# Optimization experiments

Measured on AMD Instinct MI355X. Metric: run time of the kernel, lower is better.

## Reference

```python
import jax, jax.numpy as jnp
import numpy as np

E = 1024   # embedding_size
H = 16     # num_heads
DH = E // H


def setup_inputs() -> dict:
    key = jax.random.key(0)
    ks = jax.random.split(key, 11)
    B, S = 2, 2048
    std = 0.02
    return {
        "query": jax.random.normal(ks[0], (B, S, E), jnp.float32),
        "key": jax.random.normal(ks[1], (B, S, E), jnp.float32),
        "value": jax.random.normal(ks[2], (B, S, E), jnp.float32),
        "Wq": jax.random.normal(ks[3], (E, E), jnp.float32) * std,
        "bq": jnp.zeros((E,), jnp.float32),
        "Wk": jax.random.normal(ks[4], (E, E), jnp.float32) * std,
        "bk": jnp.zeros((E,), jnp.float32),
        "Wv": jax.random.normal(ks[5], (E, E), jnp.float32) * std,
        "bv": jnp.zeros((E,), jnp.float32),
        "Wo": jax.random.normal(ks[6], (E, E), jnp.float32) * std,
        "bo": jnp.zeros((E,), jnp.float32),
    }


def _split_heads(x, B, S):
    # [B,S,E] -> [B,H,S,DH]
    return x.reshape(B, S, H, DH).transpose(0, 2, 1, 3)


def reference(query, key, value, Wq, bq, Wk, bk, Wv, bv, Wo, bo):
    B, S, _ = query.shape
    # torch Linear: y = x @ W.T + b
    q = _split_heads(query @ Wq.T + bq, B, S)
    k = _split_heads(key @ Wk.T + bk, B, key.shape[1])
    v = _split_heads(value @ Wv.T + bv, B, value.shape[1])
    # naive unscaled attention (original has no 1/sqrt(d) factor)
    scores = jnp.einsum("bhsd,bhtd->bhst", q, k)  # [B,H,S,T]
    attn = jax.nn.softmax(scores, axis=-1)
    out = jnp.einsum("bhst,bhtd->bhsd", attn, v)  # [B,H,S,DH]
    out = out.transpose(0, 2, 1, 3).reshape(B, S, E)
    return out @ Wo.T + bo
```

## Files before the change

### kernel.cpp

```cpp
#include <hip/hip_runtime.h>
#include <hip/hip_bf16.h>

constexpr int kB   = 2;
constexpr int kS   = 2048;
constexpr int kE   = 1024;
constexpr int kH   = 16;
constexpr int kDH  = 64;
constexpr int kTok = kB * kS;

constexpr float kLog2e = 1.4426950408889634f;

typedef short bf16x8 __attribute__((ext_vector_type(8)));
typedef float f32x4  __attribute__((ext_vector_type(4)));
typedef unsigned int uint2v __attribute__((ext_vector_type(2)));

__device__ __forceinline__ float bf2f(unsigned short s) {
  union { unsigned int u; float f; } c; c.u = ((unsigned int)s) << 16; return c.f;
}
__device__ __forceinline__ unsigned short f2bf(float f) {
  union { float f; unsigned int u; } c; c.f = f;
  unsigned int u = c.u;
  u += 0x7fffu + ((u >> 16) & 1u);
  return (unsigned short)(u >> 16);
}

__device__ __forceinline__ unsigned cvtpk(float lo, float hi) {
  unsigned r;
  asm("v_cvt_pk_bf16_f32 %0, %1, %2" : "=v"(r) : "v"(lo), "v"(hi));
  return r;
}

__device__ __forceinline__ float fexp2(float x) {
  float r;
  asm("v_exp_f32 %0, %1" : "=v"(r) : "v"(x));
  return r;
}

__device__ __forceinline__ void gl_lds16(const unsigned short* g, unsigned short* l) {
  __builtin_amdgcn_global_load_lds(
      (const __attribute__((address_space(1))) unsigned int*)g,
      (__attribute__((address_space(3))) unsigned int*)l, 16, 0, 0);
}

__global__ void detect_dtype(const unsigned short* __restrict__ q, int* flag) {
  __shared__ int cnt;
  if (threadIdx.x == 0) cnt = 0;
  __syncthreads();
  int bad = 0;
  for (int i = threadIdx.x; i < 4096; i += 256) {
    unsigned int e = (q[i] >> 7) & 0xFF;
    if (e >= 0xC0) bad++;
  }
  atomicAdd(&cnt, bad);
  __syncthreads();
  if (threadIdx.x == 0) *flag = (cnt > 8) ? 1 : 0;
}

struct Seg { const void* src; unsigned short* dst; unsigned int n; unsigned int blk0; };
struct ConvArgs { Seg s[11]; float scale[11]; };

__global__ __launch_bounds__(256) void conv_all(ConvArgs a, const int* __restrict__ flag) {
  const unsigned int bid = blockIdx.x;
  int si = 0;
  #pragma unroll
  for (int i = 1; i < 11; ++i)
    if (bid >= a.s[i].blk0) si = i;
  const Seg sg = a.s[si];
  const float sc = a.scale[si];
  const int i0 = ((int)(bid - sg.blk0) * 256 + threadIdx.x) * 8;
  if (i0 >= (int)sg.n) return;
  if (*flag) {
    const float* s = (const float*)sg.src + i0;
    f32x4 f0 = *(const f32x4*)(s);
    f32x4 f1 = *(const f32x4*)(s + 4);
    bf16x8 v;
    #pragma unroll
    for (int j = 0; j < 4; ++j) v[j]     = (short)f2bf(f0[j] * sc);
    #pragma unroll
    for (int j = 0; j < 4; ++j) v[j + 4] = (short)f2bf(f1[j] * sc);
    *(bf16x8*)&sg.dst[i0] = v;
  } else {
    bf16x8 v = *(const bf16x8*)((const unsigned short*)sg.src + i0);
    if (sc != 1.0f) {
      #pragma unroll
      for (int j = 0; j < 8; ++j)
        v[j] = (short)f2bf(bf2f((unsigned short)v[j]) * sc);
    }
    *(bf16x8*)&sg.dst[i0] = v;
  }
}

__device__ __forceinline__ void gemm_core(
    const unsigned short* __restrict__ A,
    const unsigned short* __restrict__ W,
    int Kdim, int bM, int bN,
    unsigned short* As, unsigned short* Ws,
    f32x4 acc[4][4])
{
  const int tid  = threadIdx.x;
  const int lane = tid & 63;
  const int wv   = tid >> 6;
  const int wm   = (wv >> 1) * 64;
  const int wn   = (wv & 1) * 64;
  const int lr   = lane & 15;
  const int kq   = (lane >> 4) * 8;

  const int r0 = tid >> 2;
  const int c0 = (tid & 3) * 8;

  const unsigned short* Ag = A + (size_t)(bM + r0) * Kdim + c0;
  const unsigned short* Wg = W + (size_t)(bN + r0) * Kdim + c0;
  unsigned short* lA = &As[tid * 8];
  unsigned short* lW = &Ws[tid * 8];

  for (int k0 = 0; k0 < Kdim; k0 += 32) {
    gl_lds16(Ag + k0,                      lA);
    gl_lds16(Ag + (size_t)64 * Kdim + k0,  lA + 2048);
    gl_lds16(Wg + k0,                      lW);
    gl_lds16(Wg + (size_t)64 * Kdim + k0,  lW + 2048);
    __syncthreads();

    bf16x8 a[4], b[4];
    #pragma unroll
    for (int i = 0; i < 4; ++i)
      a[i] = *(const bf16x8*)&As[(wm + i * 16 + lr) * 32 + kq];
    #pragma unroll
    for (int i = 0; i < 4; ++i)
      b[i] = *(const bf16x8*)&Ws[(wn + i * 16 + lr) * 32 + kq];
    #pragma unroll
    for (int i = 0; i < 4; ++i)
      #pragma unroll
      for (int j = 0; j < 4; ++j)
        acc[i][j] = __builtin_amdgcn_mfma_f32_16x16x32_bf16(a[i], b[j], acc[i][j], 0, 0, 0);
    __syncthreads();
  }
}

__global__ __launch_bounds__(256) void gemm_qkv(
    const unsigned short* __restrict__ Abase,
    const unsigned short* __restrict__ Wbase,
    const unsigned short* __restrict__ biasbase,
    unsigned short* __restrict__ Cbase)
{
  __shared__ unsigned short As[128 * 32];
  __shared__ unsigned short Ws[128 * 32];

  const int z = blockIdx.z;
  const unsigned short* A    = Abase    + (size_t)z * (kTok * kE);
  const unsigned short* W    = Wbase    + (size_t)z * (kE * kE);
  const unsigned short* bias = biasbase + (size_t)z * kE;
  unsigned short* C          = Cbase    + (size_t)z * (kTok * kE);

  const int bM = blockIdx.y * 128;
  const int bN = blockIdx.x * 128;

  f32x4 acc[4][4] = {};
  gemm_core(A, W, kE, bM, bN, As, Ws, acc);

  const int lane = threadIdx.x & 63;
  const int wv   = threadIdx.x >> 6;
  const int wm   = (wv >> 1) * 64;
  const int wn   = (wv & 1) * 64;
  const int lr   = lane & 15;
  const int qd   = lane >> 4;
  #pragma unroll
  for (int j = 0; j < 4; ++j) {
    const int col = bN + wn + j * 16 + lr;
    const float bb = bf2f(bias[col]);
    #pragma unroll
    for (int i = 0; i < 4; ++i)
      #pragma unroll
      for (int r = 0; r < 4; ++r) {
        const int row = bM + wm + i * 16 + qd * 4 + r;
        C[(size_t)row * kE + col] = f2bf(acc[i][j][r] + bb);
      }
  }
}

__global__ __launch_bounds__(256) void vtrans(
    const unsigned short* __restrict__ Vb,
    unsigned short* __restrict__ Vt)
{
  __shared__ unsigned short Lt[64 * 72];
  const int tid = threadIdx.x;
  const int bh  = blockIdx.y;
  const int b   = bh >> 4;
  const int h   = bh & 15;
  const int hcol = h * kDH;
  const int s0  = blockIdx.x * 64;

  #pragma unroll
  for (int issue = 0; issue < 2; ++issue) {
    int g = issue * 256 + tid;
    int r = g >> 3, c = (g & 7) * 8;
    bf16x8 vv = *(const bf16x8*)&Vb[(size_t)(b * kS + s0 + r) * kE + hcol + c];
    const int swz = ((((r >> 3) ^ (c >> 3)) & 7) << 3) + (r & 7);
    #pragma unroll
    for (int i = 0; i < 8; ++i)
      Lt[(c + i) * 72 + swz] = (unsigned short)vv[i];
  }
  __syncthreads();
  #pragma unroll
  for (int issue = 0; issue < 2; ++issue) {
    int g = issue * 256 + tid;
    int f = g >> 3, tc = (g & 7) * 8;
    const int blk = ((tc >> 3) ^ (f >> 3)) & 7;
    bf16x8 vv = *(const bf16x8*)&Lt[f * 72 + (blk << 3)];
    *(bf16x8*)&Vt[(size_t)b * (kE * kS) + (size_t)(hcol + f) * kS + s0 + tc] = vv;
  }
}

__global__ __launch_bounds__(256) void gemm_out(
    const unsigned short* __restrict__ A,
    const unsigned short* __restrict__ W,
    const unsigned short* __restrict__ bias,
    void* __restrict__ C,
    const int* __restrict__ flag)
{
  __shared__ unsigned short As[128 * 32];
  __shared__ unsigned short Ws[128 * 32];

  const int bM = blockIdx.y * 128;
  const int bN = blockIdx.x * 128;

  f32x4 acc[4][4] = {};
  gemm_core(A, W, kE, bM, bN, As, Ws, acc);

  const int lane = threadIdx.x & 63;
  const int wv   = threadIdx.x >> 6;
  const int wm   = (wv >> 1) * 64;
  const int wn   = (wv & 1) * 64;
  const int lr   = lane & 15;
  const int qd   = lane >> 4;
  if (*flag) {
    float* Cf = (float*)C;
    #pragma unroll
    for (int j = 0; j < 4; ++j) {
      const int col = bN + wn + j * 16 + lr;
      const float bb = bf2f(bias[col]);
      #pragma unroll
      for (int i = 0; i < 4; ++i)
        #pragma unroll
        for (int r = 0; r < 4; ++r) {
          const int row = bM + wm + i * 16 + qd * 4 + r;
          Cf[(size_t)row * kE + col] = acc[i][j][r] + bb;
        }
    }
  } else {
    unsigned short* Cb = (unsigned short*)C;
    #pragma unroll
    for (int j = 0; j < 4; ++j) {
      const int col = bN + wn + j * 16 + lr;
      const float bb = bf2f(bias[col]);
      #pragma unroll
      for (int i = 0; i < 4; ++i)
        #pragma unroll
        for (int r = 0; r < 4; ++r) {
          const int row = bM + wm + i * 16 + qd * 4 + r;
          Cb[(size_t)row * kE + col] = f2bf(acc[i][j][r] + bb);
        }
    }
  }
}

__global__ __launch_bounds__(256) void attn(
    const unsigned short* __restrict__ Qb,
    const unsigned short* __restrict__ Kb,
    const unsigned short* __restrict__ Vt,
    unsigned short* __restrict__ Ob)
{
  __shared__ unsigned short Ks[2][64 * 72];
  __shared__ unsigned short Vs[2][64 * 72];

  const int tid  = threadIdx.x;
  const int lane = tid & 63;
  const int w    = tid >> 6;
  const int lr   = lane & 15;
  const int quad = lane >> 4;
  const int kq   = quad * 8;

  const int bh = blockIdx.y;
  const int b  = bh >> 4;
  const int h  = bh & 15;
  const int q0 = blockIdx.x * 128;

  const size_t rowbase = (size_t)b * kS * kE;
  const int hcol = h * kDH;
  const unsigned short* Vbase = Vt + (size_t)b * (kE * kS) + (size_t)hcol * kS;

  const int r0 = tid >> 3;
  const int c0 = (tid & 7) * 8;

  bf16x8 aq[2][2];
  #pragma unroll
  for (int rg = 0; rg < 2; ++rg)
    #pragma unroll
    for (int hh = 0; hh < 2; ++hh)
      aq[rg][hh] = *(const bf16x8*)
          &Qb[rowbase + (size_t)(q0 + w * 32 + rg * 16 + lr) * kE + hcol + hh * 32 + kq];

  f32x4 o[2][4] = {};
  float l4[2][4] = {};

  bf16x8 rk0 = *(const bf16x8*)&Kb[rowbase + (size_t)(r0)      * kE + hcol + c0];
  bf16x8 rk1 = *(const bf16x8*)&Kb[rowbase + (size_t)(r0 + 32) * kE + hcol + c0];
  bf16x8 rv0 = *(const bf16x8*)&Vbase[(size_t)(r0)      * kS + c0];
  bf16x8 rv1 = *(const bf16x8*)&Vbase[(size_t)(r0 + 32) * kS + c0];
  *(bf16x8*)&Ks[0][ r0       * 72 + c0] = rk0;
  *(bf16x8*)&Ks[0][(r0 + 32) * 72 + c0] = rk1;
  *(bf16x8*)&Vs[0][ r0       * 72 + c0] = rv0;
  *(bf16x8*)&Vs[0][(r0 + 32) * 72 + c0] = rv1;
  rk0 = *(const bf16x8*)&Kb[rowbase + (size_t)(64 + r0)      * kE + hcol + c0];
  rk1 = *(const bf16x8*)&Kb[rowbase + (size_t)(64 + r0 + 32) * kE + hcol + c0];
  rv0 = *(const bf16x8*)&Vbase[(size_t)(r0)      * kS + 64 + c0];
  rv1 = *(const bf16x8*)&Vbase[(size_t)(r0 + 32) * kS + 64 + c0];
  __syncthreads();

  for (int t0 = 0; t0 < kS; t0 += 64) {
    const int cur = (t0 >> 6) & 1;
    const int nxt = cur ^ 1;

    if (t0 + 64 < kS) {
      *(bf16x8*)&Ks[nxt][ r0       * 72 + c0] = rk0;
      *(bf16x8*)&Ks[nxt][(r0 + 32) * 72 + c0] = rk1;
      *(bf16x8*)&Vs[nxt][ r0       * 72 + c0] = rv0;
      *(bf16x8*)&Vs[nxt][(r0 + 32) * 72 + c0] = rv1;
    }
    if (t0 + 128 < kS) {
      const int t2 = t0 + 128;
      rk0 = *(const bf16x8*)&Kb[rowbase + (size_t)(t2 + r0)      * kE + hcol + c0];
      rk1 = *(const bf16x8*)&Kb[rowbase + (size_t)(t2 + r0 + 32) * kE + hcol + c0];
      rv0 = *(const bf16x8*)&Vbase[(size_t)(r0)      * kS + t2 + c0];
      rv1 = *(const bf16x8*)&Vbase[(size_t)(r0 + 32) * kS + t2 + c0];
    }

    f32x4 s[2][4];
    #pragma unroll
    for (int rg = 0; rg < 2; ++rg)
      #pragma unroll
      for (int tn = 0; tn < 4; ++tn)
        s[rg][tn] = f32x4{0.f, 0.f, 0.f, 0.f};
    __builtin_amdgcn_s_setprio(1);
    #pragma unroll
    for (int tn = 0; tn < 4; ++tn) {
      const bf16x8 bk0 = *(const bf16x8*)&Ks[cur][(tn * 16 + lr) * 72 + 0 + kq];
      const bf16x8 bk1 = *(const bf16x8*)&Ks[cur][(tn * 16 + lr) * 72 + 32 + kq];
      #pragma unroll
      for (int rg = 0; rg < 2; ++rg) {
        s[rg][tn] = __builtin_amdgcn_mfma_f32_16x16x32_bf16(bk0, aq[rg][0], s[rg][tn], 0, 0, 0);
        s[rg][tn] = __builtin_amdgcn_mfma_f32_16x16x32_bf16(bk1, aq[rg][1], s[rg][tn], 0, 0, 0);
      }
    }
    __builtin_amdgcn_s_setprio(0);

    #pragma unroll
    for (int rg = 0; rg < 2; ++rg)
      #pragma unroll
      for (int tn = 0; tn < 4; ++tn)
        #pragma unroll
        for (int r = 0; r < 4; ++r) {
          const float e = fexp2(s[rg][tn][r]);
          s[rg][tn][r] = e;
          l4[rg][r] += e;
        }

    bf16x8 ap[2][2];
    #pragma unroll
    for (int rg = 0; rg < 2; ++rg)
      #pragma unroll
      for (int kk = 0; kk < 2; ++kk) {
        const unsigned A0 = cvtpk(s[rg][2 * kk][0],     s[rg][2 * kk][1]);
        const unsigned A1 = cvtpk(s[rg][2 * kk + 1][0], s[rg][2 * kk + 1][1]);
        const uint2v u   = __builtin_amdgcn_permlane32_swap(A0, A1, false, false);
        const uint2v z02 = __builtin_amdgcn_permlane16_swap(u[0], u[1], false, false);
        const unsigned B0 = cvtpk(s[rg][2 * kk][2],     s[rg][2 * kk][3]);
        const unsigned B1 = cvtpk(s[rg][2 * kk + 1][2], s[rg][2 * kk + 1][3]);
        const uint2v v2  = __builtin_amdgcn_permlane32_swap(B0, B1, false, false);
        const uint2v z13 = __builtin_amdgcn_permlane16_swap(v2[0], v2[1], false, false);
        union { unsigned ud[4]; bf16x8 v; } pk;
        pk.ud[0] = z02[0];
        pk.ud[1] = z13[0];
        pk.ud[2] = z02[1];
        pk.ud[3] = z13[1];
        ap[rg][kk] = pk.v;
      }

    __builtin_amdgcn_s_setprio(1);
    #pragma unroll
    for (int kk = 0; kk < 2; ++kk)
      #pragma unroll
      for (int dt = 0; dt < 4; ++dt) {
        const bf16x8 bv = *(const bf16x8*)&Vs[cur][(dt * 16 + lr) * 72 + kk * 32 + kq];
        #pragma unroll
        for (int rg = 0; rg < 2; ++rg)
          o[rg][dt] = __builtin_amdgcn_mfma_f32_16x16x32_bf16(ap[rg][kk], bv, o[rg][dt], 0, 0, 0);
      }
    __builtin_amdgcn_s_setprio(0);

    __syncthreads();
  }

  #pragma unroll
  for (int rg = 0; rg < 2; ++rg) {
    float l = (l4[rg][0] + l4[rg][1]) + (l4[rg][2] + l4[rg][3]);
    l += __shfl_xor(l, 16, 64);
    l += __shfl_xor(l, 32, 64);
    float inv[4];
    #pragma unroll
    for (int r = 0; r < 4; ++r)
      inv[r] = 1.0f / __shfl(l, quad * 4 + r, 64);

    #pragma unroll
    for (int dt = 0; dt < 4; ++dt) {
      #pragma unroll
      for (int r = 0; r < 4; ++r) {
        const int row = q0 + w * 32 + rg * 16 + quad * 4 + r;
        const int col = hcol + dt * 16 + lr;
        Ob[rowbase + (size_t)row * kE + col] = f2bf(o[rg][dt][r] * inv[r]);
      }
    }
  }
}

extern "C" void kernel_launch(void* const* d_in, const int* in_sizes, int n_in,
                              void* d_out, int out_size, void* d_ws, size_t ws_size,
                              hipStream_t stream) {
  const int nQKV = kTok * kE;
  const int nW   = kE * kE;
  const int nB   = kE;

  char* wsb = (char*)d_ws;
  int* flag = (int*)wsb;
  unsigned short* qc  = (unsigned short*)(wsb + 16);
  unsigned short* kc  = qc  + (size_t)nQKV;
  unsigned short* vc  = kc  + (size_t)nQKV;
  unsigned short* Wqc = vc  + (size_t)nQKV;
  unsigned short* Wkc = Wqc + (size_t)nW;
  unsigned short* Wvc = Wkc + (size_t)nW;
  unsigned short* Woc = Wvc + (size_t)nW;
  unsigned short* bqc = Woc + (size_t)nW;
  unsigned short* bkc = bqc + nB;
  unsigned short* bvc = bkc + nB;
  unsigned short* boc = bvc + nB;
  unsigned short* Qb  = boc + nB;
  unsigned short* Kb  = Qb  + (size_t)nQKV;
  unsigned short* Vb  = Kb  + (size_t)nQKV;
  unsigned short* Vtb = kc;
  unsigned short* Ob  = qc;

  detect_dtype<<<1, 256, 0, stream>>>((const unsigned short*)d_in[0], flag);

  ConvArgs ca;
  const void* srcs[11] = { d_in[0], d_in[1], d_in[2], d_in[3], d_in[4], d_in[5],
                           d_in[6], d_in[7], d_in[8], d_in[9], d_in[10] };
  unsigned short* dsts[11] = { qc, kc, vc, Wqc, bqc, Wkc, bkc, Wvc, bvc, Woc, boc };
  const unsigned int ns[11] = { (unsigned)nQKV, (unsigned)nQKV, (unsigned)nQKV,
                                (unsigned)nW, (unsigned)nB, (unsigned)nW, (unsigned)nB,
                                (unsigned)nW, (unsigned)nB, (unsigned)nW, (unsigned)nB };
  unsigned int blk = 0;
  for (int i = 0; i < 11; ++i) {
    ca.s[i].src = srcs[i]; ca.s[i].dst = dsts[i]; ca.s[i].n = ns[i]; ca.s[i].blk0 = blk;
    ca.scale[i] = 1.0f;
    blk += (ns[i] + 2047) / 2048;
  }
  ca.scale[3] = kLog2e;
  ca.scale[4] = kLog2e;
  conv_all<<<blk, 256, 0, stream>>>(ca, flag);

  dim3 blk256(256);
  dim3 gqkv(kE / 128, kTok / 128, 3);
  gemm_qkv<<<gqkv, blk256, 0, stream>>>(qc, Wqc, bqc, Qb);

  dim3 gvt(kS / 64, kB * kH);
  vtrans<<<gvt, blk256, 0, stream>>>(Vb, Vtb);

  dim3 gattn(kS / 128, kB * kH);
  attn<<<gattn, blk256, 0, stream>>>(Qb, Kb, Vtb, Ob);

  dim3 gout(kE / 128, kTok / 128);
  gemm_out<<<gout, blk256, 0, stream>>>(Ob, Woc, boc, d_out, flag);
}
```

Baseline: 261.7 us.

## Double-buffer GEMM LDS tiles and remap block IDs for XCD locality

The GEMM core now prefetches the next K-slice into a second LDS buffer while MFMAs run on the current one, so each step needs one barrier instead of two and global loads overlap with compute. Separately, the QKV, output-projection and attention kernels remap linear block IDs with an 8-way swizzle so blocks dispatched to the same XCD touch neighbouring tiles, aiming for better L2 reuse. This doubles LDS use per GEMM block, which may lower occupancy.

Measured after the change: 248.6 us. -5.0%, faster.

```diff
diff --git a/kernel.cpp b/kernel.cpp
--- a/kernel.cpp
+++ b/kernel.cpp
@@ -113,25 +113,35 @@
   unsigned short* lA = &As[tid * 8];
   unsigned short* lW = &Ws[tid * 8];
 
+  gl_lds16(Ag,                      lA);
+  gl_lds16(Ag + (size_t)64 * Kdim,  lA + 2048);
+  gl_lds16(Wg,                      lW);
+  gl_lds16(Wg + (size_t)64 * Kdim,  lW + 2048);
+  __syncthreads();
+
   for (int k0 = 0; k0 < Kdim; k0 += 32) {
-    gl_lds16(Ag + k0,                      lA);
-    gl_lds16(Ag + (size_t)64 * Kdim + k0,  lA + 2048);
-    gl_lds16(Wg + k0,                      lW);
-    gl_lds16(Wg + (size_t)64 * Kdim + k0,  lW + 2048);
-    __syncthreads();
+    const int co = ((k0 >> 5) & 1) * 4096;
+    if (k0 + 32 < Kdim) {
+      const int no = co ^ 4096;
+      gl_lds16(Ag + k0 + 32,                      lA + no);
+      gl_lds16(Ag + (size_t)64 * Kdim + k0 + 32,  lA + no + 2048);
+      gl_lds16(Wg + k0 + 32,                      lW + no);
+      gl_lds16(Wg + (size_t)64 * Kdim + k0 + 32,  lW + no + 2048);
+    }
 
     bf16x8 a[4], b[4];
     #pragma unroll
     for (int i = 0; i < 4; ++i)
-      a[i] = *(const bf16x8*)&As[(wm + i * 16 + lr) * 32 + kq];
+      a[i] = *(const bf16x8*)&As[co + (wm + i * 16 + lr) * 32 + kq];
     #pragma unroll
     for (int i = 0; i < 4; ++i)
-      b[i] = *(const bf16x8*)&Ws[(wn + i * 16 + lr) * 32 + kq];
+      b[i] = *(const bf16x8*)&Ws[co + (wn + i * 16 + lr) * 32 + kq];
     #pragma unroll
     for (int i = 0; i < 4; ++i)
       #pragma unroll
       for (int j = 0; j < 4; ++j)
         acc[i][j] = __builtin_amdgcn_mfma_f32_16x16x32_bf16(a[i], b[j], acc[i][j], 0, 0, 0);
+
     __syncthreads();
   }
 }
@@ -142,17 +152,20 @@
     const unsigned short* __restrict__ biasbase,
     unsigned short* __restrict__ Cbase)
 {
-  __shared__ unsigned short As[128 * 32];
-  __shared__ unsigned short Ws[128 * 32];
-
-  const int z = blockIdx.z;
+  __shared__ unsigned short As[2 * 128 * 32];
+  __shared__ unsigned short Ws[2 * 128 * 32];
+
+  const int bid = blockIdx.x + (blockIdx.y << 3) + (blockIdx.z << 8);
+  const int swz = (bid & 7) * 96 + (bid >> 3);
+  const int z   = swz >> 8;
+  const int rem = swz & 255;
+  const int bM  = (rem >> 3) * 128;
+  const int bN  = (rem & 7) * 128;
+
   const unsigned short* A    = Abase    + (size_t)z * (kTok * kE);
   const unsigned short* W    = Wbase    + (size_t)z * (kE * kE);
   const unsigned short* bias = biasbase + (size_t)z * kE;
   unsigned short* C          = Cbase    + (size_t)z * (kTok * kE);
-
-  const int bM = blockIdx.y * 128;
-  const int bN = blockIdx.x * 128;
 
   f32x4 acc[4][4] = {};
   gemm_core(A, W, kE, bM, bN, As, Ws, acc);
@@ -217,11 +230,13 @@
     void* __restrict__ C,
     const int* __restrict__ flag)
 {
-  __shared__ unsigned short As[128 * 32];
-  __shared__ unsigned short Ws[128 * 32];
-
-  const int bM = blockIdx.y * 128;
-  const int bN = blockIdx.x * 128;
+  __shared__ unsigned short As[2 * 128 * 32];
+  __shared__ unsigned short Ws[2 * 128 * 32];
+
+  const int bid = blockIdx.x + (blockIdx.y << 3);
+  const int swz = (bid & 7) * 32 + (bid >> 3);
+  const int bM  = (swz >> 3) * 128;
+  const int bN  = (swz & 7) * 128;
 
   f32x4 acc[4][4] = {};
   gemm_core(A, W, kE, bM, bN, As, Ws, acc);
@@ -279,10 +294,12 @@
   const int quad = lane >> 4;
   const int kq   = quad * 8;
 
-  const int bh = blockIdx.y;
-  const int b  = bh >> 4;
-  const int h  = bh & 15;
-  const int q0 = blockIdx.x * 128;
+  const int bid = blockIdx.x + (blockIdx.y << 4);
+  const int swz = (bid & 7) * 64 + (bid >> 3);
+  const int bh  = swz >> 4;
+  const int b   = bh >> 4;
+  const int h   = bh & 15;
+  const int q0  = (swz & 15) * 128;
 
   const size_t rowbase = (size_t)b * kS * kE;
   const int hcol = h * kDH;
```
